# Performance work log

Hardware: AMD Instinct MI355X
Metric: run time of the kernel (lower is better)

## Reference

```python
import jax, jax.numpy as jnp
import numpy as np

N = 100000
E = 1600000
NEG_SLOPE = 0.2


def _gat_layer(x, src, dst, W, a_src, a_dst, b, heads, out_ch):
    n = x.shape[0]
    h = (x @ W).reshape(n, heads, out_ch)                      # [N,H,C]
    alpha_src = (h * a_src).sum(-1)                            # [N,H]
    alpha_dst = (h * a_dst).sum(-1)                            # [N,H]
    e = jax.nn.leaky_relu(alpha_src[src] + alpha_dst[dst], NEG_SLOPE)  # [E,H]
    # segment softmax over incoming edges of each destination node
    m = jax.ops.segment_max(e, dst, num_segments=n)            # [N,H]
    ex = jnp.exp(e - m[dst])
    denom = jax.ops.segment_sum(ex, dst, num_segments=n)       # [N,H]
    alpha = ex / (denom[dst] + 1e-16)                          # [E,H]
    msg = h[src] * alpha[:, :, None]                           # [E,H,C]
    out = jax.ops.segment_sum(msg, dst, num_segments=n)        # [N,H,C]
    return out.reshape(n, heads * out_ch) + b


def setup_inputs() -> dict:
    key = jax.random.key(0)
    ks = jax.random.split(key, 10)
    glorot = lambda k, shape: jax.random.normal(k, shape, jnp.float32) * np.sqrt(2.0 / (shape[0] + shape[-1]))
    x = jax.random.normal(ks[0], (N, 5), jnp.float32)
    edge_index = jax.random.randint(ks[1], (2, E), 0, N, jnp.int64)
    return {
        "x": x,
        "edge_index": edge_index,
        "W1": glorot(ks[2], (5, 64)),
        "a_src1": glorot(ks[3], (8, 8)),
        "a_dst1": glorot(ks[4], (8, 8)),
        "b1": jnp.zeros((64,), jnp.float32),
        "W2": glorot(ks[5], (64, 2)),
        "a_src2": glorot(ks[6], (1, 2)),
        "a_dst2": glorot(ks[7], (1, 2)),
        "b2": jnp.zeros((2,), jnp.float32),
    }


def reference(x, edge_index, W1, a_src1, a_dst1, b1, W2, a_src2, a_dst2, b2):
    n = x.shape[0]
    loop = jnp.arange(n, dtype=edge_index.dtype)
    src = jnp.concatenate([edge_index[0], loop])   # PyG GATConv adds self-loops
    dst = jnp.concatenate([edge_index[1], loop])
    # dropout layers are no-ops in eval mode
    h = jax.nn.elu(_gat_layer(x, src, dst, W1, a_src1, a_dst1, b1, heads=8, out_ch=8))
    out = _gat_layer(h, src, dst, W2, a_src2, a_dst2, b2, heads=1, out_ch=2)
    return jax.nn.log_softmax(out, axis=1)
```

## Files before the change

kernel.cpp:

```cpp
#include <hip/hip_runtime.h>
#include <hip/hip_fp16.h>
#include <math.h>
#include <stdint.h>

#define N_NODES 100000
#define N_EDGES 1600000
#define N_TOT   (N_EDGES + N_NODES)
#define NEG_SLOPE 0.2f
#define LOG2E 1.44269504088896340736f

#define CB     128
#define CBBITS 7
#define NCB    ((N_NODES + CB - 1) / CB)
#define TP     2048
#define NPB    ((N_EDGES + TP - 1) / TP)
#define WINB   2560

typedef int nt_int4 __attribute__((ext_vector_type(4)));

__global__ void k_node1(const float* __restrict__ x, const float* __restrict__ W1,
                        const float* __restrict__ a_src1, const float* __restrict__ a_dst1,
                        __half* __restrict__ h1h, __half* __restrict__ as1h,
                        float* __restrict__ ad1) {
    int tid  = blockIdx.x * blockDim.x + threadIdx.x;
    int n    = tid >> 3;
    int head = tid & 7;
    if (n >= N_NODES) return;

    float xv[5];
#pragma unroll
    for (int k = 0; k < 5; ++k) xv[k] = x[n * 5 + k];

    float hv[8];
    float as = 0.f, ad = 0.f;
#pragma unroll
    for (int j = 0; j < 8; ++j) {
        int c = head * 8 + j;
        float acc = 0.f;
#pragma unroll
        for (int k = 0; k < 5; ++k) acc += xv[k] * W1[k * 64 + c];
        hv[j] = acc;
        as += acc * a_src1[c];
        ad += acc * a_dst1[c];
    }
    __half2* hp = (__half2*)&h1h[(size_t)n * 64 + head * 8];
#pragma unroll
    for (int j = 0; j < 4; ++j)
        hp[j] = __halves2half2(__float2half(hv[2 * j]), __float2half(hv[2 * j + 1]));
    as1h[n * 8 + head] = __float2half(as * LOG2E);
    ad1[n * 8 + head] = ad * LOG2E;
}

__global__ void __launch_bounds__(512) k_part(
        const int* __restrict__ src, const int* __restrict__ dst,
        int* __restrict__ ofs, unsigned* __restrict__ pairs) {
    __shared__ int lcnt[1024];
    __shared__ int sm[512];
    __shared__ unsigned stage[TP];
    int blk = blockIdx.x;
    int t = threadIdx.x;
    int base = blk * TP + t * 4;
    bool act = base < N_EDGES;
    int nE = min(TP, N_EDGES - blk * TP);

    lcnt[t] = 0; lcnt[t + 512] = 0;
    __syncthreads();

    nt_int4 s4, d4;
    if (act) {
        s4 = __builtin_nontemporal_load((const nt_int4*)(src + base));
        d4 = __builtin_nontemporal_load((const nt_int4*)(dst + base));
#pragma unroll
        for (int j = 0; j < 4; ++j) atomicAdd(&lcnt[d4[j] >> CBBITS], 1);
    }
    __syncthreads();

    int b0 = lcnt[t * 2], b1 = lcnt[t * 2 + 1];
    int local = b0 + b1;
    sm[t] = local;
    __syncthreads();
    for (int off = 1; off < 512; off <<= 1) {
        int u = (t >= off) ? sm[t - off] : 0;
        __syncthreads();
        sm[t] += u;
        __syncthreads();
    }
    int run = sm[t] - local;
    lcnt[t * 2] = run; lcnt[t * 2 + 1] = run + b0;
    int* orow = ofs + (size_t)blk * (NCB + 1);
    if (t * 2     <= NCB) orow[t * 2]     = run;
    if (t * 2 + 1 <= NCB) orow[t * 2 + 1] = run + b0;
    __syncthreads();

    if (act) {
#pragma unroll
        for (int j = 0; j < 4; ++j) {
            int d = d4[j], s = s4[j];
            int bin = d >> CBBITS;
            int idx = atomicAdd(&lcnt[bin], 1);
            stage[idx] = ((unsigned)(d & (CB - 1)) << 17) | (unsigned)s;
        }
    }
    __syncthreads();
    for (int i = t; i < nE; i += 512)
        pairs[(size_t)blk * TP + i] = stage[i];
}

__global__ void __launch_bounds__(512) k_csr(
        const int* __restrict__ ofs, const unsigned* __restrict__ pairs,
        int* __restrict__ rbeg, int* __restrict__ rend, int* __restrict__ ssrc) {
    __shared__ unsigned stIn[WINB];
    __shared__ int stOut[WINB];
    __shared__ int lcnt[CB], lofs[CB], lcur[CB];
    __shared__ int wsum[2];
    __shared__ int acur;
    int B = blockIdx.x, t = threadIdx.x;
    int nvalid = min(CB, N_NODES - B * CB);
    int obase = B * WINB;

    if (t < CB) {
        lcnt[t] = (t < nvalid) ? 1 : 0;
        lcur[t] = 1;
    }
    if (t == 0) acur = 0;
    __syncthreads();

    for (int blk = t; blk < NPB; blk += 512) {
        int o0 = ofs[(size_t)blk * (NCB + 1) + B];
        int o1 = ofs[(size_t)blk * (NCB + 1) + B + 1];
        int n = o1 - o0;
        if (n > 0) {
            int p = atomicAdd(&acur, n);
            const unsigned* pp = pairs + (size_t)blk * TP + o0;
            for (int i = 0; i < n; ++i) {
                unsigned r = pp[i];
                stIn[p + i] = r;
                atomicAdd(&lcnt[r >> 17], 1);
            }
        }
    }
    __syncthreads();
    int m = acur;

    int v = (t < CB) ? lcnt[t] : 0;
    int ln = t & 63, wv = t >> 6;
    int sc = v;
#pragma unroll
    for (int off = 1; off < 64; off <<= 1) {
        int u = __shfl_up(sc, off, 64);
        if (ln >= off) sc += u;
    }
    if (ln == 63 && wv < 2) wsum[wv] = sc;
    __syncthreads();
    int wbase = (wv == 1) ? wsum[0] : 0;
    int ex = wbase + sc - v;
    if (t < CB) {
        lofs[t] = ex;
        int gi = B * CB + t;
        if (gi < N_NODES) {
            rbeg[gi] = obase + ex;
            rend[gi] = obase + ex + v;
            stOut[ex] = gi;
        }
    }
    __syncthreads();

    for (int k = t; k < m; k += 512) {
        unsigned p = stIn[k];
        int dl = p >> 17;
        int idx = atomicAdd(&lcur[dl], 1);
        stOut[lofs[dl] + idx] = (int)(p & 0x1FFFF);
    }
    __syncthreads();

    int tot = m + nvalid;
    for (int i = t; i < tot; i += 512) ssrc[obase + i] = stOut[i];
}

__global__ void __launch_bounds__(256) k_gather1(
        const int* __restrict__ rbeg, const int* __restrict__ rend,
        const int* __restrict__ ssrc, const float4* __restrict__ h1x4,
        const __half* __restrict__ as1h, const float* __restrict__ ad1,
        const float* __restrict__ b1, const float* __restrict__ W2,
        const float* __restrict__ a_src2, const float* __restrict__ a_dst2,
        float4* __restrict__ rec) {
    int gtid = blockIdx.x * blockDim.x + threadIdx.x;
    int d    = gtid >> 6;
    int lane = threadIdx.x & 63;
    if (d >= N_NODES) return;
    int e = lane >> 3;
    int h = lane & 7;

    int beg = rbeg[d], end = rend[d];
    float adv = ad1[d * 8 + h];
    float a0 = 0.f, a1 = 0.f, a2 = 0.f, a3 = 0.f;
    float a4 = 0.f, a5 = 0.f, a6 = 0.f, a7 = 0.f, den = 0.f;

    int k = beg;
    for (; k + 16 <= end; k += 16) {
        int sA = ssrc[k + e];
        int sB = ssrc[k + 8 + e];
        float eA = __half2float(as1h[sA * 8 + h]);
        float eB = __half2float(as1h[sB * 8 + h]);
        float4 rA = h1x4[(size_t)sA * 8 + h];
        float4 rB = h1x4[(size_t)sB * 8 + h];
        float tA = eA + adv; tA = fmaxf(tA, NEG_SLOPE * tA);
        float tB = eB + adv; tB = fmaxf(tB, NEG_SLOPE * tB);
        float wA = __builtin_amdgcn_exp2f(tA);
        float wB = __builtin_amdgcn_exp2f(tB);
        float2 fA0 = __half22float2(*(__half2*)&rA.x);
        float2 fA1 = __half22float2(*(__half2*)&rA.y);
        float2 fA2 = __half22float2(*(__half2*)&rA.z);
        float2 fA3 = __half22float2(*(__half2*)&rA.w);
        float2 fB0 = __half22float2(*(__half2*)&rB.x);
        float2 fB1 = __half22float2(*(__half2*)&rB.y);
        float2 fB2 = __half22float2(*(__half2*)&rB.z);
        float2 fB3 = __half22float2(*(__half2*)&rB.w);
        a0 += wA * fA0.x + wB * fB0.x;
        a1 += wA * fA0.y + wB * fB0.y;
        a2 += wA * fA1.x + wB * fB1.x;
        a3 += wA * fA1.y + wB * fB1.y;
        a4 += wA * fA2.x + wB * fB2.x;
        a5 += wA * fA2.y + wB * fB2.y;
        a6 += wA * fA3.x + wB * fB3.x;
        a7 += wA * fA3.y + wB * fB3.y;
        den += wA + wB;
    }
    for (; k < end; k += 8) {
        int ki = k + e;
        bool val = ki < end;
        int s = ssrc[val ? ki : beg];
        float ev = __half2float(as1h[s * 8 + h]);
        float4 r = h1x4[(size_t)s * 8 + h];
        float t = ev + adv; t = fmaxf(t, NEG_SLOPE * t);
        float w = val ? __builtin_amdgcn_exp2f(t) : 0.f;
        float2 f0 = __half22float2(*(__half2*)&r.x);
        float2 f1 = __half22float2(*(__half2*)&r.y);
        float2 f2 = __half22float2(*(__half2*)&r.z);
        float2 f3 = __half22float2(*(__half2*)&r.w);
        a0 += w * f0.x; a1 += w * f0.y;
        a2 += w * f1.x; a3 += w * f1.y;
        a4 += w * f2.x; a5 += w * f2.y;
        a6 += w * f3.x; a7 += w * f3.y;
        den += w;
    }

#define RED8(x) x += __shfl_xor(x, 8, 64); x += __shfl_xor(x, 16, 64); x += __shfl_xor(x, 32, 64);
    RED8(a0) RED8(a1) RED8(a2) RED8(a3)
    RED8(a4) RED8(a5) RED8(a6) RED8(a7)
    RED8(den)
#undef RED8

    float inv = 1.f / den;
    float4 b01 = ((const float4*)b1)[2 * h];
    float4 b23 = ((const float4*)b1)[2 * h + 1];
    float v0 = a0 * inv + b01.x;
    float v1 = a1 * inv + b01.y;
    float v2 = a2 * inv + b01.z;
    float v3 = a3 * inv + b01.w;
    float v4 = a4 * inv + b23.x;
    float v5 = a5 * inv + b23.y;
    float v6 = a6 * inv + b23.z;
    float v7 = a7 * inv + b23.w;
    v0 = (v0 > 0.f) ? v0 : (__expf(v0) - 1.f);
    v1 = (v1 > 0.f) ? v1 : (__expf(v1) - 1.f);
    v2 = (v2 > 0.f) ? v2 : (__expf(v2) - 1.f);
    v3 = (v3 > 0.f) ? v3 : (__expf(v3) - 1.f);
    v4 = (v4 > 0.f) ? v4 : (__expf(v4) - 1.f);
    v5 = (v5 > 0.f) ? v5 : (__expf(v5) - 1.f);
    v6 = (v6 > 0.f) ? v6 : (__expf(v6) - 1.f);
    v7 = (v7 > 0.f) ? v7 : (__expf(v7) - 1.f);

    const float4* w4 = (const float4*)(W2 + h * 16);
    float4 wq0 = w4[0], wq1 = w4[1], wq2 = w4[2], wq3 = w4[3];
    float h20 = v0 * wq0.x + v1 * wq0.z + v2 * wq1.x + v3 * wq1.z
              + v4 * wq2.x + v5 * wq2.z + v6 * wq3.x + v7 * wq3.z;
    float h21 = v0 * wq0.y + v1 * wq0.w + v2 * wq1.y + v3 * wq1.w
              + v4 * wq2.y + v5 * wq2.w + v6 * wq3.y + v7 * wq3.w;
    h20 += __shfl_xor(h20, 1, 64); h20 += __shfl_xor(h20, 2, 64); h20 += __shfl_xor(h20, 4, 64);
    h21 += __shfl_xor(h21, 1, 64); h21 += __shfl_xor(h21, 2, 64); h21 += __shfl_xor(h21, 4, 64);

    if (lane == 0) {
        float as2v = h20 * a_src2[0] + h21 * a_src2[1];
        float ad2v = h20 * a_dst2[0] + h21 * a_dst2[1];
        rec[d] = make_float4(h20, h21, as2v, ad2v);
    }
}

__global__ void k_gather2(const int* __restrict__ rbeg, const int* __restrict__ rend,
                          const int* __restrict__ ssrc, const float4* __restrict__ rec,
                          const float* __restrict__ b2, float* __restrict__ out) {
    int gtid = blockIdx.x * blockDim.x + threadIdx.x;
    int d    = gtid >> 4;
    int lane = gtid & 15;
    if (d >= N_NODES) return;

    int beg = rbeg[d], end = rend[d];
    float adv = rec[d].w;
    float n0 = 0.f, n1 = 0.f, den = 0.f;
    int k = beg + lane;
    for (; k + 16 < end; k += 32) {
        int s0 = ssrc[k], s1 = ssrc[k + 16];
        float4 r0 = rec[s0];
        float4 r1 = rec[s1];
        float t0 = r0.z + adv; t0 = fmaxf(t0, NEG_SLOPE * t0);
        float t1 = r1.z + adv; t1 = fmaxf(t1, NEG_SLOPE * t1);
        float w0 = __expf(t0), w1 = __expf(t1);
        n0 += w0 * r0.x + w1 * r1.x;
        n1 += w0 * r0.y + w1 * r1.y;
        den += w0 + w1;
    }
    if (k < end) {
        int s = ssrc[k];
        float4 r = rec[s];
        float t = r.z + adv; t = fmaxf(t, NEG_SLOPE * t);
        float w = __expf(t);
        n0 += w * r.x; n1 += w * r.y; den += w;
    }
#pragma unroll
    for (int off = 8; off; off >>= 1) {
        n0  += __shfl_xor(n0,  off, 16);
        n1  += __shfl_xor(n1,  off, 16);
        den += __shfl_xor(den, off, 16);
    }
    if (lane == 0) {
        float o0 = n0 / den + b2[0];
        float o1 = n1 / den + b2[1];
        float m  = fmaxf(o0, o1);
        float lse = m + __logf(__expf(o0 - m) + __expf(o1 - m));
        out[d * 2 + 0] = o0 - lse;
        out[d * 2 + 1] = o1 - lse;
    }
}

extern "C" void kernel_launch(void* const* d_in, const int* in_sizes, int n_in,
                              void* d_out, int out_size, void* d_ws, size_t ws_size,
                              hipStream_t stream) {
    const float* x      = (const float*)d_in[0];
    const int*   ei     = (const int*)d_in[1];
    const float* W1     = (const float*)d_in[2];
    const float* a_src1 = (const float*)d_in[3];
    const float* a_dst1 = (const float*)d_in[4];
    const float* b1     = (const float*)d_in[5];
    const float* W2     = (const float*)d_in[6];
    const float* a_src2 = (const float*)d_in[7];
    const float* a_dst2 = (const float*)d_in[8];
    const float* b2     = (const float*)d_in[9];
    float* out = (float*)d_out;

    const int* src = ei;
    const int* dst = ei + N_EDGES;

    int* ofs    = (int*)d_ws;
    int* rbeg   = ofs + (size_t)NPB * (NCB + 1);
    int* rend   = rbeg + N_NODES;
    unsigned* pairs = (unsigned*)(rend + N_NODES);
    int* ssrc   = (int*)(pairs + N_EDGES);
    uintptr_t pp = ((uintptr_t)(ssrc + (size_t)NCB * WINB) + 255) & ~(uintptr_t)255;
    float4*   rec  = (float4*)pp;
    float*    ad1  = (float*)(rec + N_NODES);
    __half*   h1h  = (__half*)(ad1 + (size_t)N_NODES * 8);
    __half*   as1h = h1h + (size_t)N_NODES * 64;

    k_node1<<<(N_NODES * 8 + 255) / 256, 256, 0, stream>>>(x, W1, a_src1, a_dst1,
                                                           h1h, as1h, ad1);
    k_part<<<NPB, 512, 0, stream>>>(src, dst, ofs, pairs);
    k_csr<<<NCB, 512, 0, stream>>>(ofs, pairs, rbeg, rend, ssrc);
    k_gather1<<<(N_NODES * 64 + 255) / 256, 256, 0, stream>>>(rbeg, rend, ssrc,
                                                              (const float4*)h1h,
                                                              as1h, ad1, b1, W2,
                                                              a_src2, a_dst2, rec);
    k_gather2<<<(N_NODES * 16 + 255) / 256, 256, 0, stream>>>(rbeg, rend, ssrc,
                                                              rec, b2, out);
}
```

Before: 181.2 us.

## Aggregate raw 5-dim inputs per head then apply W1 after softmax

Because the layer-1 projection is linear, the gather now accumulates attention-weighted 5-channel input features (stored as padded fp16, 16 bytes per node) and multiplies by W1 once per destination node after normalisation. This replaces per-edge gathers of 64-channel fp16 projected features (128 bytes per node), shrinking the random-access gather footprint and the workspace. It adds a small per-node matrix-vector product. Each lane still loads the whole 16-byte row, so the 8 head lanes of an edge now read the same address.

```diff
diff --git a/kernel.cpp b/kernel.cpp
--- a/kernel.cpp
+++ b/kernel.cpp
@@ -20,7 +20,7 @@
 
 __global__ void k_node1(const float* __restrict__ x, const float* __restrict__ W1,
                         const float* __restrict__ a_src1, const float* __restrict__ a_dst1,
-                        __half* __restrict__ h1h, __half* __restrict__ as1h,
+                        __half* __restrict__ xh, __half* __restrict__ as1h,
                         float* __restrict__ ad1) {
     int tid  = blockIdx.x * blockDim.x + threadIdx.x;
     int n    = tid >> 3;
@@ -31,7 +31,6 @@
 #pragma unroll
     for (int k = 0; k < 5; ++k) xv[k] = x[n * 5 + k];
 
-    float hv[8];
     float as = 0.f, ad = 0.f;
 #pragma unroll
     for (int j = 0; j < 8; ++j) {
@@ -39,16 +38,20 @@
         float acc = 0.f;
 #pragma unroll
         for (int k = 0; k < 5; ++k) acc += xv[k] * W1[k * 64 + c];
-        hv[j] = acc;
         as += acc * a_src1[c];
         ad += acc * a_dst1[c];
     }
-    __half2* hp = (__half2*)&h1h[(size_t)n * 64 + head * 8];
-#pragma unroll
-    for (int j = 0; j < 4; ++j)
-        hp[j] = __halves2half2(__float2half(hv[2 * j]), __float2half(hv[2 * j + 1]));
     as1h[n * 8 + head] = __float2half(as * LOG2E);
     ad1[n * 8 + head] = ad * LOG2E;
+
+    if (head == 0) {
+        __half2 p0 = __halves2half2(__float2half(xv[0]), __float2half(xv[1]));
+        __half2 p1 = __halves2half2(__float2half(xv[2]), __float2half(xv[3]));
+        __half2 p2 = __halves2half2(__float2half(xv[4]), __float2half(0.f));
+        __half2 p3 = __halves2half2(__float2half(0.f), __float2half(0.f));
+        __half2* xp = (__half2*)&xh[(size_t)n * 8];
+        xp[0] = p0; xp[1] = p1; xp[2] = p2; xp[3] = p3;
+    }
 }
 
 __global__ void __launch_bounds__(512) k_part(
@@ -179,9 +182,10 @@
 
 __global__ void __launch_bounds__(256) k_gather1(
         const int* __restrict__ rbeg, const int* __restrict__ rend,
-        const int* __restrict__ ssrc, const float4* __restrict__ h1x4,
+        const int* __restrict__ ssrc, const float4* __restrict__ xh4,
         const __half* __restrict__ as1h, const float* __restrict__ ad1,
-        const float* __restrict__ b1, const float* __restrict__ W2,
+        const float* __restrict__ b1, const float* __restrict__ W1,
+        const float* __restrict__ W2,
         const float* __restrict__ a_src2, const float* __restrict__ a_dst2,
         float4* __restrict__ rec) {
     int gtid = blockIdx.x * blockDim.x + threadIdx.x;
@@ -193,8 +197,7 @@
 
     int beg = rbeg[d], end = rend[d];
     float adv = ad1[d * 8 + h];
-    float a0 = 0.f, a1 = 0.f, a2 = 0.f, a3 = 0.f;
-    float a4 = 0.f, a5 = 0.f, a6 = 0.f, a7 = 0.f, den = 0.f;
+    float c0 = 0.f, c1 = 0.f, c2 = 0.f, c3 = 0.f, c4 = 0.f, den = 0.f;
 
     int k = beg;
     for (; k + 16 <= end; k += 16) {
@@ -202,28 +205,23 @@
         int sB = ssrc[k + 8 + e];
         float eA = __half2float(as1h[sA * 8 + h]);
         float eB = __half2float(as1h[sB * 8 + h]);
-        float4 rA = h1x4[(size_t)sA * 8 + h];
-        float4 rB = h1x4[(size_t)sB * 8 + h];
+        float4 xA = xh4[sA];
+        float4 xB = xh4[sB];
         float tA = eA + adv; tA = fmaxf(tA, NEG_SLOPE * tA);
         float tB = eB + adv; tB = fmaxf(tB, NEG_SLOPE * tB);
         float wA = __builtin_amdgcn_exp2f(tA);
         float wB = __builtin_amdgcn_exp2f(tB);
-        float2 fA0 = __half22float2(*(__half2*)&rA.x);
-        float2 fA1 = __half22float2(*(__half2*)&rA.y);
-        float2 fA2 = __half22float2(*(__half2*)&rA.z);
-        float2 fA3 = __half22float2(*(__half2*)&rA.w);
-        float2 fB0 = __half22float2(*(__half2*)&rB.x);
-        float2 fB1 = __half22float2(*(__half2*)&rB.y);
-        float2 fB2 = __half22float2(*(__half2*)&rB.z);
-        float2 fB3 = __half22float2(*(__half2*)&rB.w);
-        a0 += wA * fA0.x + wB * fB0.x;
-        a1 += wA * fA0.y + wB * fB0.y;
-        a2 += wA * fA1.x + wB * fB1.x;
-        a3 += wA * fA1.y + wB * fB1.y;
-        a4 += wA * fA2.x + wB * fB2.x;
-        a5 += wA * fA2.y + wB * fB2.y;
-        a6 += wA * fA3.x + wB * fB3.x;
-        a7 += wA * fA3.y + wB * fB3.y;
+        float2 A01 = __half22float2(*(__half2*)&xA.x);
+        float2 A23 = __half22float2(*(__half2*)&xA.y);
+        float2 A4_ = __half22float2(*(__half2*)&xA.z);
+        float2 B01 = __half22float2(*(__half2*)&xB.x);
+        float2 B23 = __half22float2(*(__half2*)&xB.y);
+        float2 B4_ = __half22float2(*(__half2*)&xB.z);
+        c0 += wA * A01.x + wB * B01.x;
+        c1 += wA * A01.y + wB * B01.y;
+        c2 += wA * A23.x + wB * B23.x;
+        c3 += wA * A23.y + wB * B23.y;
+        c4 += wA * A4_.x + wB * B4_.x;
         den += wA + wB;
     }
     for (; k < end; k += 8) {
@@ -231,37 +229,39 @@
         bool val = ki < end;
         int s = ssrc[val ? ki : beg];
         float ev = __half2float(as1h[s * 8 + h]);
-        float4 r = h1x4[(size_t)s * 8 + h];
+        float4 xr = xh4[s];
         float t = ev + adv; t = fmaxf(t, NEG_SLOPE * t);
         float w = val ? __builtin_amdgcn_exp2f(t) : 0.f;
-        float2 f0 = __half22float2(*(__half2*)&r.x);
-        float2 f1 = __half22float2(*(__half2*)&r.y);
-        float2 f2 = __half22float2(*(__half2*)&r.z);
-        float2 f3 = __half22float2(*(__half2*)&r.w);
-        a0 += w * f0.x; a1 += w * f0.y;
-        a2 += w * f1.x; a3 += w * f1.y;
-        a4 += w * f2.x; a5 += w * f2.y;
-        a6 += w * f3.x; a7 += w * f3.y;
+        float2 X01 = __half22float2(*(__half2*)&xr.x);
+        float2 X23 = __half22float2(*(__half2*)&xr.y);
+        float2 X4_ = __half22float2(*(__half2*)&xr.z);
+        c0 += w * X01.x; c1 += w * X01.y;
+        c2 += w * X23.x; c3 += w * X23.y;
+        c4 += w * X4_.x;
         den += w;
     }
 
 #define RED8(x) x += __shfl_xor(x, 8, 64); x += __shfl_xor(x, 16, 64); x += __shfl_xor(x, 32, 64);
-    RED8(a0) RED8(a1) RED8(a2) RED8(a3)
-    RED8(a4) RED8(a5) RED8(a6) RED8(a7)
-    RED8(den)
+    RED8(c0) RED8(c1) RED8(c2) RED8(c3) RED8(c4) RED8(den)
 #undef RED8
 
     float inv = 1.f / den;
-    float4 b01 = ((const float4*)b1)[2 * h];
-    float4 b23 = ((const float4*)b1)[2 * h + 1];
-    float v0 = a0 * inv + b01.x;
-    float v1 = a1 * inv + b01.y;
-    float v2 = a2 * inv + b01.z;
-    float v3 = a3 * inv + b01.w;
-    float v4 = a4 * inv + b23.x;
-    float v5 = a5 * inv + b23.y;
-    float v6 = a6 * inv + b23.z;
-    float v7 = a7 * inv + b23.w;
+    float s0 = c0 * inv, s1 = c1 * inv, s2 = c2 * inv,
+          s3 = c3 * inv, s4 = c4 * inv;
+
+    float4 hA = ((const float4*)b1)[2 * h];
+    float4 hB = ((const float4*)b1)[2 * h + 1];
+#pragma unroll
+    for (int c = 0; c < 5; ++c) {
+        float xc = (c == 0) ? s0 : (c == 1) ? s1 : (c == 2) ? s2
+                 : (c == 3) ? s3 : s4;
+        float4 wA = *(const float4*)(W1 + c * 64 + 8 * h);
+        float4 wB = *(const float4*)(W1 + c * 64 + 8 * h + 4);
+        hA.x += xc * wA.x; hA.y += xc * wA.y; hA.z += xc * wA.z; hA.w += xc * wA.w;
+        hB.x += xc * wB.x; hB.y += xc * wB.y; hB.z += xc * wB.z; hB.w += xc * wB.w;
+    }
+    float v0 = hA.x, v1 = hA.y, v2 = hA.z, v3 = hA.w;
+    float v4 = hB.x, v5 = hB.y, v6 = hB.z, v7 = hB.w;
     v0 = (v0 > 0.f) ? v0 : (__expf(v0) - 1.f);
     v1 = (v1 > 0.f) ? v1 : (__expf(v1) - 1.f);
     v2 = (v2 > 0.f) ? v2 : (__expf(v2) - 1.f);
@@ -359,16 +359,16 @@
     uintptr_t pp = ((uintptr_t)(ssrc + (size_t)NCB * WINB) + 255) & ~(uintptr_t)255;
     float4*   rec  = (float4*)pp;
     float*    ad1  = (float*)(rec + N_NODES);
-    __half*   h1h  = (__half*)(ad1 + (size_t)N_NODES * 8);
-    __half*   as1h = h1h + (size_t)N_NODES * 64;
+    __half*   as1h = (__half*)(ad1 + (size_t)N_NODES * 8);
+    __half*   xh   = as1h + (size_t)N_NODES * 8;
 
     k_node1<<<(N_NODES * 8 + 255) / 256, 256, 0, stream>>>(x, W1, a_src1, a_dst1,
-                                                           h1h, as1h, ad1);
+                                                           xh, as1h, ad1);
     k_part<<<NPB, 512, 0, stream>>>(src, dst, ofs, pairs);
     k_csr<<<NCB, 512, 0, stream>>>(ofs, pairs, rbeg, rend, ssrc);
     k_gather1<<<(N_NODES * 64 + 255) / 256, 256, 0, stream>>>(rbeg, rend, ssrc,
-                                                              (const float4*)h1h,
-                                                              as1h, ad1, b1, W2,
+                                                              (const float4*)xh,
+                                                              as1h, ad1, b1, W1, W2,
                                                               a_src2, a_dst2, rec);
     k_gather2<<<(N_NODES * 16 + 255) / 256, 256, 0, stream>>>(rbeg, rend, ssrc,
                                                               rec, b2, out);
```

Result: slower. 199.0 us (+9.8%).
